# Optimization experiments

Measured on AMD Instinct MI355X. Metric: run time of the kernel, lower is better.

The kernel has to match this reference:

```python
import jax, jax.numpy as jnp
import numpy as np

N_IN, N_OUT, H, EMB, NSC = 32, 8, 256, 32, 5
B, T = 256, 512
D_IN0 = N_IN + N_OUT + EMB  # 72


def setup_inputs() -> dict:
    key = jax.random.key(0)
    ks = jax.random.split(key, 18)
    s = 0.05
    rn = lambda k, shape: (jax.random.normal(k, shape, jnp.float32) * s)
    return {
        "x_cv": jax.random.normal(ks[0], (B, T, N_IN), jnp.float32),
        "pv_init": jax.random.normal(ks[1], (B, N_OUT), jnp.float32),
        "scenario": jax.random.randint(ks[2], (B,), 0, NSC),
        "emb_table": rn(ks[3], (NSC, EMB)),
        "W_ih0": rn(ks[4], (4 * H, D_IN0)),
        "W_hh0": rn(ks[5], (4 * H, H)),
        "b_ih0": rn(ks[6], (4 * H,)),
        "b_hh0": rn(ks[7], (4 * H,)),
        "W_ih1": rn(ks[8], (4 * H, H)),
        "W_hh1": rn(ks[9], (4 * H, H)),
        "b_ih1": rn(ks[10], (4 * H,)),
        "b_hh1": rn(ks[11], (4 * H,)),
        "fc1_w": rn(ks[12], (H // 2, H)),
        "fc1_b": rn(ks[13], (H // 2,)),
        "fc2_w": rn(ks[14], (N_OUT, H // 2)),
        "fc2_b": rn(ks[15], (N_OUT,)),
    }


def _lstm_cell(x, h, c, W_ih, W_hh, b):
    # torch gate order: i, f, g, o
    g = x @ W_ih.T + h @ W_hh.T + b
    i, f, gg, o = jnp.split(g, 4, axis=-1)
    c_new = jax.nn.sigmoid(f) * c + jax.nn.sigmoid(i) * jnp.tanh(gg)
    h_new = jax.nn.sigmoid(o) * jnp.tanh(c_new)
    return h_new, c_new


def reference(x_cv, pv_init, scenario, emb_table, W_ih0, W_hh0, b_ih0, b_hh0,
              W_ih1, W_hh1, b_ih1, b_hh1, fc1_w, fc1_b, fc2_w, fc2_b):
    # previous prediction. Dropout inactive (eval mode).
    emb = emb_table[scenario]          # [B, EMB]
    b0 = b_ih0 + b_hh0
    b1 = b_ih1 + b_hh1
    Bsz = x_cv.shape[0]
    z = jnp.zeros((Bsz, H), x_cv.dtype)

    def step(carry, x_t):
        h0, c0, h1, c1, pv = carry
        xt = jnp.concatenate([x_t, pv, emb], axis=-1)   # [B, D_IN0]
        h0, c0 = _lstm_cell(xt, h0, c0, W_ih0, W_hh0, b0)
        h1, c1 = _lstm_cell(h0, h1, c1, W_ih1, W_hh1, b1)
        pv_pred = jax.nn.relu(h1 @ fc1_w.T + fc1_b) @ fc2_w.T + fc2_b
        new_carry = (h0, c0, h1, c1, jax.lax.stop_gradient(pv_pred))
        return new_carry, pv_pred

    init = (z, z, z, z, pv_init)
    _, outs = jax.lax.scan(step, init, jnp.swapaxes(x_cv, 0, 1))  # [T, B, N_OUT]
    return jnp.swapaxes(outs, 0, 1)  # [B, T, N_OUT]
```

## Files before the change

kernel.cpp:

```cpp
#include <hip/hip_runtime.h>
#include <hip/hip_bf16.h>


#define TSTEPS 512

typedef _Float16 h2 __attribute__((ext_vector_type(2)));
typedef unsigned long long ull;

#if __has_builtin(__builtin_amdgcn_fdot2)
#define FDOT2(a, b, c) __builtin_amdgcn_fdot2((a), (b), (c), false)
#else
#define FDOT2(a, b, c) ((c) + (float)(a).x * (float)(b).x + (float)(a).y * (float)(b).y)
#endif
#define BC(x) __builtin_bit_cast(h2, (x))

__device__ __forceinline__ float sigm(float x) { return 1.0f / (1.0f + __expf(-x)); }
__device__ __forceinline__ float tanhf_(float x) {
    float e = __expf(2.0f * x);
    return 1.0f - 2.0f / (e + 1.0f);
}

#define WQT_OFF 0u
#define HXA_OFF 1703936u
#define HXB_OFF 1966080u
#define FLG_OFF 2228224u
#define WS_NEED 2244608u

__device__ __forceinline__ float l0col(const float* __restrict__ Wih0,
                                       const float* __restrict__ Whh0, int row, int K) {
    if (K < 32) return Wih0[row * 72 + K];
    if (K < 288) return Whh0[row * 256 + (K - 32)];
    if (K < 296) return Wih0[row * 72 + 32 + (K - 288)];
    return 0.0f;
}

__global__ void prep_w(const float* __restrict__ Wih0, const float* __restrict__ Whh0,
                       const float* __restrict__ Wih1, const float* __restrict__ Whh1,
                       char* __restrict__ ws) {
    int gid = blockIdx.x * 256 + threadIdx.x;
    if (gid < 106496) {
        int q = gid % 52;
        int rest = gid / 52;
        int l = rest & 63, w = (rest >> 6) & 7, c = rest >> 9;
        float4 v;
        float* vp = (float*)&v;
#pragma unroll
        for (int gg = 0; gg < 4; ++gg) {
            int row = gg * 256 + c * 64 + l;
            float a0, a1;
            if (q < 20) {
                int K = w * 40 + q * 2;
                a0 = l0col(Wih0, Whh0, row, K);
                a1 = l0col(Wih0, Whh0, row, K + 1);
            } else if (q < 36) {
                int K = w * 32 + (q - 20) * 2;
                a0 = Wih1[row * 256 + K];
                a1 = Wih1[row * 256 + K + 1];
            } else {
                int K = w * 32 + (q - 36) * 2;
                a0 = Whh1[row * 256 + K];
                a1 = Whh1[row * 256 + K + 1];
            }
            h2 hv;
            hv.x = (_Float16)a0;
            hv.y = (_Float16)a1;
            vp[gg] = __builtin_bit_cast(float, hv);
        }
        ((float4*)ws)[gid] = v;
    } else {
        int z = gid - 106496;
        if (z < 4096) ((unsigned*)(ws + FLG_OFF))[z] = 0u;
    }
}

__device__ __forceinline__ void arrive(unsigned* cnt) {
    asm volatile("s_waitcnt vmcnt(0)" ::: "memory");
    __hip_atomic_fetch_add(cnt, 1u, __ATOMIC_RELAXED, __HIP_MEMORY_SCOPE_AGENT);
}
__device__ __forceinline__ void wait_cnt(unsigned* cnt, unsigned tgt) {
    while (__hip_atomic_load(cnt, __ATOMIC_RELAXED, __HIP_MEMORY_SCOPE_AGENT) < tgt)
        __builtin_amdgcn_s_sleep(1);
}
#define CBAR() asm volatile("" ::: "memory")

__device__ __forceinline__ void mac4(const float4& W, h2 x, float& r0, float& r1,
                                     float& r2, float& r3) {
    r0 = FDOT2(BC(W.x), x, r0);
    r1 = FDOT2(BC(W.y), x, r1);
    r2 = FDOT2(BC(W.z), x, r2);
    r3 = FDOT2(BC(W.w), x, r3);
}
__device__ __forceinline__ float dot8(const float4& W, const float4& X, float s) {
    s = FDOT2(BC(W.x), BC(X.x), s);
    s = FDOT2(BC(W.y), BC(X.y), s);
    s = FDOT2(BC(W.z), BC(X.z), s);
    s = FDOT2(BC(W.w), BC(X.w), s);
    return s;
}

__global__ __launch_bounds__(512) void lstm_main(
    const float* __restrict__ x_cv, const float* __restrict__ pv_init,
    const int* __restrict__ scen, const float* __restrict__ emb_table,
    const float* __restrict__ Wih0, const float* __restrict__ b_ih0,
    const float* __restrict__ b_hh0, const float* __restrict__ b_ih1,
    const float* __restrict__ b_hh1, const float* __restrict__ fc1_w,
    const float* __restrict__ fc1_b, const float* __restrict__ fc2_w,
    const float* __restrict__ fc2_b, char* __restrict__ ws,
    float* __restrict__ out) {
    struct __align__(16) SM {
        char fc1w[73856];
        char fc2w[2048];
        char xt0[4 * 640];
        char xt1[4 * 1024];
        float g0[4][256];
        float g1[4][256];
        float biasE[4][256];
        float bias1[256];
        unsigned short htmp[4][64];
        char fc1o[4 * 256];
        float embs[4][32];
        int scen_l[4];
    };
    __shared__ SM sm;

    const int tid = threadIdx.x;
    const int lane = tid & 63;
    const int wv = tid >> 6;
    const int c = blockIdx.x & 3;
    const int g = blockIdx.x >> 2;
    const int B0 = g * 4;

    ull* hxA = (ull*)(ws + HXA_OFF) + (unsigned)g * 512u;
    ull* hxB = (ull*)(ws + HXB_OFF) + (unsigned)g * 512u;
    unsigned* cntA = (unsigned*)(ws + FLG_OFF) + (unsigned)g * 32u;
    unsigned* cntB = cntA + 16;

    float4 wr[52];
    {
        const float4* wb = (const float4*)(ws + WQT_OFF) +
                           (unsigned)(((c * 8 + wv) * 64 + lane) * 52);
#pragma unroll
        for (int q = 0; q < 52; ++q) wr[q] = wb[q];
    }

    if (tid < 4) sm.scen_l[tid] = scen[B0 + tid];
    __syncthreads();

    if (tid < 128) {
        int b = tid >> 5, e = tid & 31;
        sm.embs[b][e] = emb_table[sm.scen_l[b] * 32 + e];
    }
    if (tid < 320) ((ull*)sm.xt0)[tid] = 0ull;
    ((ull*)sm.xt1)[tid] = 0ull;
    {
        int ks = tid & 3, row = tid >> 2;
        char* dst = sm.fc1w + ks * 18464 + row * 144;
        const float* src = fc1_w + row * 256 + ks * 64;
        for (int e = 0; e < 32; ++e) {
            h2 v;
            v.x = (_Float16)src[2 * e];
            v.y = (_Float16)src[2 * e + 1];
            *(h2*)(dst + e * 4) = v;
        }
    }
    {
        int jo = tid >> 6, ks = (tid >> 4) & 3, e = tid & 15;
        h2 v;
        v.x = (_Float16)fc2_w[jo * 128 + ks * 32 + 2 * e];
        v.y = (_Float16)fc2_w[jo * 128 + ks * 32 + 2 * e + 1];
        *(h2*)(sm.fc2w + (jo * 4 + ks) * 64 + e * 4) = v;
    }
    if (tid < 256) {
        int row = (tid >> 6) * 256 + c * 64 + (tid & 63);
        sm.bias1[tid] = b_ih1[row] + b_hh1[row];
    }
    __syncthreads();

    for (int idx = tid; idx < 1024; idx += 512) {
        int b = idx >> 8, r = idx & 255;
        int row = (r >> 6) * 256 + c * 64 + (r & 63);
        float s = b_ih0[row] + b_hh0[row];
        for (int e = 0; e < 32; ++e) s += sm.embs[b][e] * Wih0[row * 72 + 40 + e];
        sm.biasE[b][r] = s;
    }
    if (tid < 128) {
        int b = tid >> 5, k = tid & 31;
        float xv = x_cv[((size_t)(B0 + b) * TSTEPS + 0) * 32 + k];
        *(_Float16*)(sm.xt0 + b * 640 + k * 2) = (_Float16)xv;
    }
    if (tid < 32) {
        int b = tid >> 3, jo = tid & 7;
        *(_Float16*)(sm.xt0 + b * 640 + 576 + jo * 2) = (_Float16)pv_init[(B0 + b) * 8 + jo];
    }
    __syncthreads();

    for (int idx = tid; idx < 1024; idx += 512) {
        int b = idx >> 8, r = idx & 255;
        sm.g0[b][r] = sm.biasE[b][r];
        sm.g1[b][r] = sm.bias1[r];
    }
    const float fc1b_r = fc1_b[tid >> 2];
    const float fc2b_r = (tid < 128) ? fc2_b[(tid >> 2) & 7] : 0.0f;
    float c0 = 0.0f, c1 = 0.0f;
    __syncthreads();

    for (int t = 0; t < TSTEPS; ++t) {
        const int par = t & 1;
        const unsigned tgt = 4u * (unsigned)(t + 1);

        {
            float a0[4], a1[4], a2[4], a3[4];
#pragma unroll
            for (int b = 0; b < 4; ++b) a0[b] = a1[b] = a2[b] = a3[b] = 0.0f;
#pragma unroll
            for (int b = 0; b < 4; ++b) {
                const char* xb = sm.xt0 + b * 640 + wv * 80;
#pragma unroll
                for (int q = 0; q < 5; ++q) {
                    float4 xq = *(const float4*)(xb + q * 16);
                    mac4(wr[q * 4 + 0], BC(xq.x), a0[b], a1[b], a2[b], a3[b]);
                    mac4(wr[q * 4 + 1], BC(xq.y), a0[b], a1[b], a2[b], a3[b]);
                    mac4(wr[q * 4 + 2], BC(xq.z), a0[b], a1[b], a2[b], a3[b]);
                    mac4(wr[q * 4 + 3], BC(xq.w), a0[b], a1[b], a2[b], a3[b]);
                }
            }
#pragma unroll
            for (int b = 0; b < 4; ++b) {
                atomicAdd(&sm.g0[b][lane], a0[b]);
                atomicAdd(&sm.g0[b][64 + lane], a1[b]);
                atomicAdd(&sm.g0[b][128 + lane], a2[b]);
                atomicAdd(&sm.g0[b][192 + lane], a3[b]);
            }
        }
        __syncthreads();

        if (tid < 256) {
            int u = tid & 63, b = tid >> 6;
            float gi = sm.g0[b][u], gf = sm.g0[b][64 + u];
            float gc = sm.g0[b][128 + u], go = sm.g0[b][192 + u];
            c0 = sigm(gf) * c0 + sigm(gi) * tanhf_(gc);
            float h = sigm(go) * tanhf_(c0);
            sm.htmp[b][u] = __builtin_bit_cast(unsigned short, (_Float16)h);
        }
        __syncthreads();

        float b0a[4], b1a[4], b2a[4], b3a[4];
        if (wv == 0) {
            ull v = *(const ull*)((const char*)sm.htmp +
                                  ((lane >> 4) * 64 + (lane & 15) * 4) * 2);
            __hip_atomic_store(&hxA[(par * 4 + c) * 64 + lane], v, __ATOMIC_RELAXED,
                               __HIP_MEMORY_SCOPE_AGENT);
            if (lane == 0) arrive(cntA);
        }
        {
#pragma unroll
            for (int b = 0; b < 4; ++b) b0a[b] = b1a[b] = b2a[b] = b3a[b] = 0.0f;
#pragma unroll
            for (int b = 0; b < 4; ++b) {
                const char* xb = sm.xt1 + b * 1024 + 512 + wv * 64;
#pragma unroll
                for (int q = 0; q < 4; ++q) {
                    float4 xq = *(const float4*)(xb + q * 16);
                    mac4(wr[36 + q * 4 + 0], BC(xq.x), b0a[b], b1a[b], b2a[b], b3a[b]);
                    mac4(wr[36 + q * 4 + 1], BC(xq.y), b0a[b], b1a[b], b2a[b], b3a[b]);
                    mac4(wr[36 + q * 4 + 2], BC(xq.z), b0a[b], b1a[b], b2a[b], b3a[b]);
                    mac4(wr[36 + q * 4 + 3], BC(xq.w), b0a[b], b1a[b], b2a[b], b3a[b]);
                }
            }
        }
        for (int idx = tid; idx < 1024; idx += 512) {
            int b = idx >> 8, r = idx & 255;
            sm.g0[b][r] = sm.biasE[b][r];
        }
        if (tid == 0) wait_cnt(cntA, tgt);
        __syncthreads();
        CBAR();

        if (tid < 256) {
            int cc = tid >> 6, l = tid & 63;
            ull v = __hip_atomic_load(&hxA[(par * 4 + cc) * 64 + l], __ATOMIC_RELAXED,
                                      __HIP_MEMORY_SCOPE_AGENT);
            int b = l >> 4, ug = cc * 64 + (l & 15) * 4;
            *(ull*)(sm.xt1 + b * 1024 + ug * 2) = v;
            *(ull*)(sm.xt0 + b * 640 + 64 + ug * 2) = v;
        }
        __syncthreads();

        {
#pragma unroll
            for (int b = 0; b < 4; ++b) {
                const char* xb = sm.xt1 + b * 1024 + wv * 64;
#pragma unroll
                for (int q = 0; q < 4; ++q) {
                    float4 xq = *(const float4*)(xb + q * 16);
                    mac4(wr[20 + q * 4 + 0], BC(xq.x), b0a[b], b1a[b], b2a[b], b3a[b]);
                    mac4(wr[20 + q * 4 + 1], BC(xq.y), b0a[b], b1a[b], b2a[b], b3a[b]);
                    mac4(wr[20 + q * 4 + 2], BC(xq.z), b0a[b], b1a[b], b2a[b], b3a[b]);
                    mac4(wr[20 + q * 4 + 3], BC(xq.w), b0a[b], b1a[b], b2a[b], b3a[b]);
                }
            }
#pragma unroll
            for (int b = 0; b < 4; ++b) {
                atomicAdd(&sm.g1[b][lane], b0a[b]);
                atomicAdd(&sm.g1[b][64 + lane], b1a[b]);
                atomicAdd(&sm.g1[b][128 + lane], b2a[b]);
                atomicAdd(&sm.g1[b][192 + lane], b3a[b]);
            }
        }
        __syncthreads();

        if (tid < 256) {
            int u = tid & 63, b = tid >> 6;
            float gi = sm.g1[b][u], gf = sm.g1[b][64 + u];
            float gc = sm.g1[b][128 + u], go = sm.g1[b][192 + u];
            c1 = sigm(gf) * c1 + sigm(gi) * tanhf_(gc);
            float h = sigm(go) * tanhf_(c1);
            sm.htmp[b][u] = __builtin_bit_cast(unsigned short, (_Float16)h);
        }
        __syncthreads();

        if (wv == 0) {
            ull v = *(const ull*)((const char*)sm.htmp +
                                  ((lane >> 4) * 64 + (lane & 15) * 4) * 2);
            __hip_atomic_store(&hxB[(par * 4 + c) * 64 + lane], v, __ATOMIC_RELAXED,
                               __HIP_MEMORY_SCOPE_AGENT);
            if (lane == 0) arrive(cntB);
        }
        if (tid >= 128 && tid < 256 && t + 1 < TSTEPS) {
            int tt = tid - 128;
            int b = tt >> 5, k = tt & 31;
            float xv = x_cv[((size_t)(B0 + b) * TSTEPS + t + 1) * 32 + k];
            *(_Float16*)(sm.xt0 + b * 640 + k * 2) = (_Float16)xv;
        }
        for (int idx = tid; idx < 1024; idx += 512) {
            int b = idx >> 8, r = idx & 255;
            sm.g1[b][r] = sm.bias1[r];
        }
        if (tid == 0) wait_cnt(cntB, tgt);
        __syncthreads();
        CBAR();

        if (tid < 256) {
            int cc = tid >> 6, l = tid & 63;
            ull v = __hip_atomic_load(&hxB[(par * 4 + cc) * 64 + l], __ATOMIC_RELAXED,
                                      __HIP_MEMORY_SCOPE_AGENT);
            int b = l >> 4, ug = cc * 64 + (l & 15) * 4;
            *(ull*)(sm.xt1 + b * 1024 + 512 + ug * 2) = v;
        }
        __syncthreads();

        {
            const int fks = tid & 3, frow = tid >> 2;
            const char* wbase = sm.fc1w + fks * 18464 + frow * 144;
            float fa[4];
#pragma unroll
            for (int b = 0; b < 4; ++b) fa[b] = 0.0f;
#pragma unroll
            for (int b = 0; b < 4; ++b) {
                const char* xb = sm.xt1 + b * 1024 + 512 + fks * 128;
#pragma unroll
                for (int q = 0; q < 8; ++q) {
                    float4 W = *(const float4*)(wbase + q * 16);
                    float4 X = *(const float4*)(xb + q * 16);
                    fa[b] = dot8(W, X, fa[b]);
                }
            }
#pragma unroll
            for (int b = 0; b < 4; ++b) {
                float s = fa[b];
                s += __shfl_xor(s, 1);
                s += __shfl_xor(s, 2);
                if (fks == 0) {
                    float r = fmaxf(s + fc1b_r, 0.0f);
                    *(unsigned short*)(sm.fc1o + b * 256 + frow * 2) =
                        __builtin_bit_cast(unsigned short, (_Float16)r);
                }
            }
        }
        __syncthreads();

        if (tid < 128) {
            int ks = tid & 3, jo = (tid >> 2) & 7, b = tid >> 5;
            const char* wb2 = sm.fc2w + (jo * 4 + ks) * 64;
            const char* xb2 = sm.fc1o + b * 256 + ks * 64;
            float s = 0.0f;
#pragma unroll
            for (int q = 0; q < 4; ++q) {
                float4 W = *(const float4*)(wb2 + q * 16);
                float4 X = *(const float4*)(xb2 + q * 16);
                s = dot8(W, X, s);
            }
            s += __shfl_xor(s, 1);
            s += __shfl_xor(s, 2);
            if (ks == 0) {
                float pv = s + fc2b_r;
                *(_Float16*)(sm.xt0 + b * 640 + 576 + jo * 2) = (_Float16)pv;
                if (c == 0) out[((size_t)(B0 + b) * TSTEPS + t) * 8 + jo] = pv;
            }
        }
        __syncthreads();
    }
}

extern "C" void kernel_launch(void* const* d_in, const int* in_sizes, int n_in,
                              void* d_out, int out_size, void* d_ws, size_t ws_size,
                              hipStream_t stream) {
    if (ws_size < WS_NEED) return;

    const float* x_cv = (const float*)d_in[0];
    const float* pv_init = (const float*)d_in[1];
    const int* scen = (const int*)d_in[2];
    const float* embt = (const float*)d_in[3];
    const float* Wih0 = (const float*)d_in[4];
    const float* Whh0 = (const float*)d_in[5];
    const float* bih0 = (const float*)d_in[6];
    const float* bhh0 = (const float*)d_in[7];
    const float* Wih1 = (const float*)d_in[8];
    const float* Whh1 = (const float*)d_in[9];
    const float* bih1 = (const float*)d_in[10];
    const float* bhh1 = (const float*)d_in[11];
    const float* fc1w = (const float*)d_in[12];
    const float* fc1b = (const float*)d_in[13];
    const float* fc2w = (const float*)d_in[14];
    const float* fc2b = (const float*)d_in[15];

    char* ws = (char*)d_ws;

    prep_w<<<432, 256, 0, stream>>>(Wih0, Whh0, Wih1, Whh1, ws);

    lstm_main<<<256, 512, 0, stream>>>(x_cv, pv_init, scen, embt, Wih0, bih0, bhh0,
                                       bih1, bhh1, fc1w, fc1b, fc2w, fc2b, ws,
                                       (float*)d_out);
}
```

Baseline: 19.10 ms.

## Repartition LSTM across 8 blocks per batch group of 8 samples

Changes the grid decomposition from 4 hidden-unit slices times 4 samples per group to 8 slices of 32 units times 8 samples per group. Each thread now keeps half as many weight registers (26 float4 instead of 52) and computes packed dot8 products over 8 samples. fc1 weights are also cached in registers with a rotated index to avoid LDS bank conflicts. The goal is to cut register pressure and raise per-weight reuse, at the cost of a wider cross-block exchange (8 blocks per barrier) and more LDS atomics per step.

```diff
diff --git a/kernel.cpp b/kernel.cpp
--- a/kernel.cpp
+++ b/kernel.cpp
@@ -24,7 +24,7 @@
 #define HXA_OFF 1703936u
 #define HXB_OFF 1966080u
 #define FLG_OFF 2228224u
-#define WS_NEED 2244608u
+#define WS_NEED 2232320u
 
 __device__ __forceinline__ float l0col(const float* __restrict__ Wih0,
                                        const float* __restrict__ Whh0, int row, int K) {
@@ -39,37 +39,48 @@
                        char* __restrict__ ws) {
     int gid = blockIdx.x * 256 + threadIdx.x;
     if (gid < 106496) {
-        int q = gid % 52;
-        int rest = gid / 52;
+        int q = gid % 26;
+        int rest = gid / 26;
         int l = rest & 63, w = (rest >> 6) & 7, c = rest >> 9;
+        int gp = l >> 5, u = l & 31;
+        int r, K;
+        const float* base = nullptr;
+        if (q < 10) {
+            r = q / 5;
+            K = w * 40 + (q % 5) * 8;
+        } else if (q < 18) {
+            int z = q - 10;
+            r = z >> 2;
+            K = w * 32 + (z & 3) * 8;
+            base = Wih1;
+        } else {
+            int z = q - 18;
+            r = z >> 2;
+            K = w * 32 + (z & 3) * 8;
+            base = Whh1;
+        }
+        int row = (gp * 2 + r) * 256 + c * 32 + u;
         float4 v;
         float* vp = (float*)&v;
 #pragma unroll
-        for (int gg = 0; gg < 4; ++gg) {
-            int row = gg * 256 + c * 64 + l;
+        for (int e = 0; e < 4; ++e) {
             float a0, a1;
-            if (q < 20) {
-                int K = w * 40 + q * 2;
-                a0 = l0col(Wih0, Whh0, row, K);
-                a1 = l0col(Wih0, Whh0, row, K + 1);
-            } else if (q < 36) {
-                int K = w * 32 + (q - 20) * 2;
-                a0 = Wih1[row * 256 + K];
-                a1 = Wih1[row * 256 + K + 1];
+            if (base) {
+                a0 = base[row * 256 + K + 2 * e];
+                a1 = base[row * 256 + K + 2 * e + 1];
             } else {
-                int K = w * 32 + (q - 36) * 2;
-                a0 = Whh1[row * 256 + K];
-                a1 = Whh1[row * 256 + K + 1];
+                a0 = l0col(Wih0, Whh0, row, K + 2 * e);
+                a1 = l0col(Wih0, Whh0, row, K + 2 * e + 1);
             }
             h2 hv;
             hv.x = (_Float16)a0;
             hv.y = (_Float16)a1;
-            vp[gg] = __builtin_bit_cast(float, hv);
+            vp[e] = __builtin_bit_cast(float, hv);
         }
         ((float4*)ws)[gid] = v;
     } else {
         int z = gid - 106496;
-        if (z < 4096) ((unsigned*)(ws + FLG_OFF))[z] = 0u;
+        if (z < 1024) ((unsigned*)(ws + FLG_OFF))[z] = 0u;
     }
 }
 
@@ -83,13 +94,6 @@
 }
 #define CBAR() asm volatile("" ::: "memory")
 
-__device__ __forceinline__ void mac4(const float4& W, h2 x, float& r0, float& r1,
-                                     float& r2, float& r3) {
-    r0 = FDOT2(BC(W.x), x, r0);
-    r1 = FDOT2(BC(W.y), x, r1);
-    r2 = FDOT2(BC(W.z), x, r2);
-    r3 = FDOT2(BC(W.w), x, r3);
-}
 __device__ __forceinline__ float dot8(const float4& W, const float4& X, float s) {
     s = FDOT2(BC(W.x), BC(X.x), s);
     s = FDOT2(BC(W.y), BC(X.y), s);
@@ -98,7 +102,7 @@
     return s;
 }
 
-__global__ __launch_bounds__(512) void lstm_main(
+__global__ __launch_bounds__(512, 2) void lstm_main(
     const float* __restrict__ x_cv, const float* __restrict__ pv_init,
     const int* __restrict__ scen, const float* __restrict__ emb_table,
     const float* __restrict__ Wih0, const float* __restrict__ b_ih0,
@@ -108,294 +112,282 @@
     const float* __restrict__ fc2_b, char* __restrict__ ws,
     float* __restrict__ out) {
     struct __align__(16) SM {
-        char fc1w[73856];
+        char fc1w[4 * 16400];
         char fc2w[2048];
-        char xt0[4 * 640];
-        char xt1[4 * 1024];
-        float g0[4][256];
-        float g1[4][256];
-        float biasE[4][256];
-        float bias1[256];
-        unsigned short htmp[4][64];
-        char fc1o[4 * 256];
-        float embs[4][32];
-        int scen_l[4];
+        char xt0[8 * 640];
+        char xt1[8 * 1024];
+        float g0[8][128];
+        float g1[8][128];
+        float biasE[8][128];
+        float bias1[128];
+        unsigned short htmp[8][32];
+        char fc1o[8 * 256];
+        float embs[8][32];
+        int scen_l[8];
     };
     __shared__ SM sm;
 
     const int tid = threadIdx.x;
     const int lane = tid & 63;
     const int wv = tid >> 6;
-    const int c = blockIdx.x & 3;
-    const int g = blockIdx.x >> 2;
-    const int B0 = g * 4;
-
-    ull* hxA = (ull*)(ws + HXA_OFF) + (unsigned)g * 512u;
-    ull* hxB = (ull*)(ws + HXB_OFF) + (unsigned)g * 512u;
+    const int c = blockIdx.x & 7;
+    const int g = blockIdx.x >> 3;
+    const int B0 = g * 8;
+    const int gp = lane >> 5, u = lane & 31;
+
+    ull* hxA = (ull*)(ws + HXA_OFF) + (unsigned)g * 1024u;
+    ull* hxB = (ull*)(ws + HXB_OFF) + (unsigned)g * 1024u;
     unsigned* cntA = (unsigned*)(ws + FLG_OFF) + (unsigned)g * 32u;
     unsigned* cntB = cntA + 16;
 
-    float4 wr[52];
+    float4 wr[26];
     {
         const float4* wb = (const float4*)(ws + WQT_OFF) +
-                           (unsigned)(((c * 8 + wv) * 64 + lane) * 52);
-#pragma unroll
-        for (int q = 0; q < 52; ++q) wr[q] = wb[q];
-    }
-
-    if (tid < 4) sm.scen_l[tid] = scen[B0 + tid];
+                           (unsigned)(((c * 8 + wv) * 64 + lane) * 26);
+#pragma unroll
+        for (int q = 0; q < 26; ++q) wr[q] = wb[q];
+    }
+
+    if (tid < 8) sm.scen_l[tid] = scen[B0 + tid];
     __syncthreads();
-
-    if (tid < 128) {
+    if (tid < 256) {
         int b = tid >> 5, e = tid & 31;
         sm.embs[b][e] = emb_table[sm.scen_l[b] * 32 + e];
     }
-    if (tid < 320) ((ull*)sm.xt0)[tid] = 0ull;
-    ((ull*)sm.xt1)[tid] = 0ull;
+    for (int idx = tid; idx < 640; idx += 512) ((ull*)sm.xt0)[idx] = 0ull;
+    for (int idx = tid; idx < 1024; idx += 512) ((ull*)sm.xt1)[idx] = 0ull;
     {
         int ks = tid & 3, row = tid >> 2;
-        char* dst = sm.fc1w + ks * 18464 + row * 144;
-        const float* src = fc1_w + row * 256 + ks * 64;
-        for (int e = 0; e < 32; ++e) {
-            h2 v;
-            v.x = (_Float16)src[2 * e];
-            v.y = (_Float16)src[2 * e + 1];
-            *(h2*)(dst + e * 4) = v;
-        }
-    }
-    {
-        int jo = tid >> 6, ks = (tid >> 4) & 3, e = tid & 15;
-        h2 v;
-        v.x = (_Float16)fc2_w[jo * 128 + ks * 32 + 2 * e];
-        v.y = (_Float16)fc2_w[jo * 128 + ks * 32 + 2 * e + 1];
-        *(h2*)(sm.fc2w + (jo * 4 + ks) * 64 + e * 4) = v;
-    }
-    if (tid < 256) {
-        int row = (tid >> 6) * 256 + c * 64 + (tid & 63);
+        for (int q = 0; q < 8; ++q) {
+            const float* src = fc1_w + row * 256 + ks * 64 + q * 8;
+            char* dst = sm.fc1w + ks * 16400 + q * 2048 + row * 16;
+#pragma unroll
+            for (int e = 0; e < 4; ++e) {
+                h2 v;
+                v.x = (_Float16)src[2 * e];
+                v.y = (_Float16)src[2 * e + 1];
+                *(h2*)(dst + e * 4) = v;
+            }
+        }
+    }
+    if (tid < 128) {
+        int jo = tid >> 4, ks = (tid >> 2) & 3, e4 = tid & 3;
+        float4 v;
+        float* vp = (float*)&v;
+#pragma unroll
+        for (int e = 0; e < 4; ++e) {
+            h2 hv;
+            hv.x = (_Float16)fc2_w[jo * 128 + ks * 32 + e4 * 8 + 2 * e];
+            hv.y = (_Float16)fc2_w[jo * 128 + ks * 32 + e4 * 8 + 2 * e + 1];
+            vp[e] = __builtin_bit_cast(float, hv);
+        }
+        *(float4*)(sm.fc2w + (jo * 4 + ks) * 64 + e4 * 16) = v;
+    }
+    if (tid < 128) {
+        int row = (tid >> 5) * 256 + c * 32 + (tid & 31);
         sm.bias1[tid] = b_ih1[row] + b_hh1[row];
     }
     __syncthreads();
-
     for (int idx = tid; idx < 1024; idx += 512) {
-        int b = idx >> 8, r = idx & 255;
-        int row = (r >> 6) * 256 + c * 64 + (r & 63);
+        int b = idx >> 7, r = idx & 127;
+        int row = (r >> 5) * 256 + c * 32 + (r & 31);
         float s = b_ih0[row] + b_hh0[row];
         for (int e = 0; e < 32; ++e) s += sm.embs[b][e] * Wih0[row * 72 + 40 + e];
         sm.biasE[b][r] = s;
     }
-    if (tid < 128) {
+    if (tid < 256) {
         int b = tid >> 5, k = tid & 31;
         float xv = x_cv[((size_t)(B0 + b) * TSTEPS + 0) * 32 + k];
         *(_Float16*)(sm.xt0 + b * 640 + k * 2) = (_Float16)xv;
     }
-    if (tid < 32) {
+    if (tid < 64) {
         int b = tid >> 3, jo = tid & 7;
         *(_Float16*)(sm.xt0 + b * 640 + 576 + jo * 2) = (_Float16)pv_init[(B0 + b) * 8 + jo];
     }
     __syncthreads();
-
     for (int idx = tid; idx < 1024; idx += 512) {
-        int b = idx >> 8, r = idx & 255;
+        int b = idx >> 7, r = idx & 127;
         sm.g0[b][r] = sm.biasE[b][r];
         sm.g1[b][r] = sm.bias1[r];
     }
-    const float fc1b_r = fc1_b[tid >> 2];
-    const float fc2b_r = (tid < 128) ? fc2_b[(tid >> 2) & 7] : 0.0f;
+    const int f_ks = tid & 3, f_row = tid >> 2;
+    const float fc1b_r = fc1_b[f_row];
+    const int ks2 = tid & 3, jo = (tid >> 2) & 7, bo = tid >> 5;
+    const float fc2b_r = (tid < 256) ? fc2_b[jo] : 0.0f;
+    float4 f1w[8];
+#pragma unroll
+    for (int i = 0; i < 8; ++i) {
+        int qx = (i + 2 * f_ks) & 7;
+        f1w[i] = *(const float4*)(sm.fc1w + f_ks * 16400 + qx * 2048 + f_row * 16);
+    }
     float c0 = 0.0f, c1 = 0.0f;
     __syncthreads();
 
     for (int t = 0; t < TSTEPS; ++t) {
         const int par = t & 1;
-        const unsigned tgt = 4u * (unsigned)(t + 1);
-
-        {
-            float a0[4], a1[4], a2[4], a3[4];
-#pragma unroll
-            for (int b = 0; b < 4; ++b) a0[b] = a1[b] = a2[b] = a3[b] = 0.0f;
-#pragma unroll
-            for (int b = 0; b < 4; ++b) {
+        const unsigned tgt = 8u * (unsigned)(t + 1);
+
+        {
+            float a0[8], a1[8];
+#pragma unroll
+            for (int b = 0; b < 8; ++b) a0[b] = a1[b] = 0.0f;
+#pragma unroll
+            for (int b = 0; b < 8; ++b) {
                 const char* xb = sm.xt0 + b * 640 + wv * 80;
 #pragma unroll
                 for (int q = 0; q < 5; ++q) {
                     float4 xq = *(const float4*)(xb + q * 16);
-                    mac4(wr[q * 4 + 0], BC(xq.x), a0[b], a1[b], a2[b], a3[b]);
-                    mac4(wr[q * 4 + 1], BC(xq.y), a0[b], a1[b], a2[b], a3[b]);
-                    mac4(wr[q * 4 + 2], BC(xq.z), a0[b], a1[b], a2[b], a3[b]);
-                    mac4(wr[q * 4 + 3], BC(xq.w), a0[b], a1[b], a2[b], a3[b]);
+                    a0[b] = dot8(wr[q], xq, a0[b]);
+                    a1[b] = dot8(wr[5 + q], xq, a1[b]);
                 }
             }
 #pragma unroll
-            for (int b = 0; b < 4; ++b) {
-                atomicAdd(&sm.g0[b][lane], a0[b]);
-                atomicAdd(&sm.g0[b][64 + lane], a1[b]);
-                atomicAdd(&sm.g0[b][128 + lane], a2[b]);
-                atomicAdd(&sm.g0[b][192 + lane], a3[b]);
+            for (int b = 0; b < 8; ++b) {
+                atomicAdd(&sm.g0[b][gp * 64 + u], a0[b]);
+                atomicAdd(&sm.g0[b][gp * 64 + 32 + u], a1[b]);
             }
         }
         __syncthreads();
 
         if (tid < 256) {
-            int u = tid & 63, b = tid >> 6;
-            float gi = sm.g0[b][u], gf = sm.g0[b][64 + u];
-            float gc = sm.g0[b][128 + u], go = sm.g0[b][192 + u];
+            int uu = tid & 31, b = tid >> 5;
+            float gi = sm.g0[b][uu], gf = sm.g0[b][32 + uu];
+            float gc = sm.g0[b][64 + uu], go = sm.g0[b][96 + uu];
             c0 = sigm(gf) * c0 + sigm(gi) * tanhf_(gc);
-            float h = sigm(go) * tanhf_(c0);
-            sm.htmp[b][u] = __builtin_bit_cast(unsigned short, (_Float16)h);
-        }
-        __syncthreads();
-
-        float b0a[4], b1a[4], b2a[4], b3a[4];
+            sm.htmp[b][uu] = __builtin_bit_cast(unsigned short, (_Float16)(sigm(go) * tanhf_(c0)));
+        }
+        __syncthreads();
+
+        float e0[8], e1[8];
         if (wv == 0) {
-            ull v = *(const ull*)((const char*)sm.htmp +
-                                  ((lane >> 4) * 64 + (lane & 15) * 4) * 2);
-            __hip_atomic_store(&hxA[(par * 4 + c) * 64 + lane], v, __ATOMIC_RELAXED,
+            ull v = ((const ull*)sm.htmp)[lane];
+            __hip_atomic_store(&hxA[(par * 8 + c) * 64 + lane], v, __ATOMIC_RELAXED,
                                __HIP_MEMORY_SCOPE_AGENT);
             if (lane == 0) arrive(cntA);
         }
         {
 #pragma unroll
-            for (int b = 0; b < 4; ++b) b0a[b] = b1a[b] = b2a[b] = b3a[b] = 0.0f;
-#pragma unroll
-            for (int b = 0; b < 4; ++b) {
+            for (int b = 0; b < 8; ++b) e0[b] = e1[b] = 0.0f;
+#pragma unroll
+            for (int b = 0; b < 8; ++b) {
                 const char* xb = sm.xt1 + b * 1024 + 512 + wv * 64;
 #pragma unroll
                 for (int q = 0; q < 4; ++q) {
                     float4 xq = *(const float4*)(xb + q * 16);
-                    mac4(wr[36 + q * 4 + 0], BC(xq.x), b0a[b], b1a[b], b2a[b], b3a[b]);
-                    mac4(wr[36 + q * 4 + 1], BC(xq.y), b0a[b], b1a[b], b2a[b], b3a[b]);
-                    mac4(wr[36 + q * 4 + 2], BC(xq.z), b0a[b], b1a[b], b2a[b], b3a[b]);
-                    mac4(wr[36 + q * 4 + 3], BC(xq.w), b0a[b], b1a[b], b2a[b], b3a[b]);
+                    e0[b] = dot8(wr[18 + q], xq, e0[b]);
+                    e1[b] = dot8(wr[22 + q], xq, e1[b]);
                 }
             }
         }
         for (int idx = tid; idx < 1024; idx += 512) {
-            int b = idx >> 8, r = idx & 255;
+            int b = idx >> 7, r = idx & 127;
             sm.g0[b][r] = sm.biasE[b][r];
         }
         if (tid == 0) wait_cnt(cntA, tgt);
         __syncthreads();
         CBAR();
 
-        if (tid < 256) {
+        {
             int cc = tid >> 6, l = tid & 63;
-            ull v = __hip_atomic_load(&hxA[(par * 4 + cc) * 64 + l], __ATOMIC_RELAXED,
+            ull v = __hip_atomic_load(&hxA[(par * 8 + cc) * 64 + l], __ATOMIC_RELAXED,
                                       __HIP_MEMORY_SCOPE_AGENT);
-            int b = l >> 4, ug = cc * 64 + (l & 15) * 4;
-            *(ull*)(sm.xt1 + b * 1024 + ug * 2) = v;
-            *(ull*)(sm.xt0 + b * 640 + 64 + ug * 2) = v;
-        }
-        __syncthreads();
-
-        {
-#pragma unroll
-            for (int b = 0; b < 4; ++b) {
+            int b = l >> 3, u4 = cc * 32 + (l & 7) * 4;
+            *(ull*)(sm.xt1 + b * 1024 + u4 * 2) = v;
+            *(ull*)(sm.xt0 + b * 640 + 64 + u4 * 2) = v;
+        }
+        __syncthreads();
+
+        {
+#pragma unroll
+            for (int b = 0; b < 8; ++b) {
                 const char* xb = sm.xt1 + b * 1024 + wv * 64;
 #pragma unroll
                 for (int q = 0; q < 4; ++q) {
                     float4 xq = *(const float4*)(xb + q * 16);
-                    mac4(wr[20 + q * 4 + 0], BC(xq.x), b0a[b], b1a[b], b2a[b], b3a[b]);
-                    mac4(wr[20 + q * 4 + 1], BC(xq.y), b0a[b], b1a[b], b2a[b], b3a[b]);
-                    mac4(wr[20 + q * 4 + 2], BC(xq.z), b0a[b], b1a[b], b2a[b], b3a[b]);
-                    mac4(wr[20 + q * 4 + 3], BC(xq.w), b0a[b], b1a[b], b2a[b], b3a[b]);
+                    e0[b] = dot8(wr[10 + q], xq, e0[b]);
+                    e1[b] = dot8(wr[14 + q], xq, e1[b]);
                 }
             }
 #pragma unroll
-            for (int b = 0; b < 4; ++b) {
-                atomicAdd(&sm.g1[b][lane], b0a[b]);
-                atomicAdd(&sm.g1[b][64 + lane], b1a[b]);
-                atomicAdd(&sm.g1[b][128 + lane], b2a[b]);
-                atomicAdd(&sm.g1[b][192 + lane], b3a[b]);
+            for (int b = 0; b < 8; ++b) {
+                atomicAdd(&sm.g1[b][gp * 64 + u], e0[b]);
+                atomicAdd(&sm.g1[b][gp * 64 + 32 + u], e1[b]);
             }
         }
         __syncthreads();
 
         if (tid < 256) {
-            int u = tid & 63, b = tid >> 6;
-            float gi = sm.g1[b][u], gf = sm.g1[b][64 + u];
-            float gc = sm.g1[b][128 + u], go = sm.g1[b][192 + u];
+            int uu = tid & 31, b = tid >> 5;
+            float gi = sm.g1[b][uu], gf = sm.g1[b][32 + uu];
+            float gc = sm.g1[b][64 + uu], go = sm.g1[b][96 + uu];
             c1 = sigm(gf) * c1 + sigm(gi) * tanhf_(gc);
-            float h = sigm(go) * tanhf_(c1);
-            sm.htmp[b][u] = __builtin_bit_cast(unsigned short, (_Float16)h);
+            sm.htmp[b][uu] = __builtin_bit_cast(unsigned short, (_Float16)(sigm(go) * tanhf_(c1)));
         }
         __syncthreads();
 
         if (wv == 0) {
-            ull v = *(const ull*)((const char*)sm.htmp +
-                                  ((lane >> 4) * 64 + (lane & 15) * 4) * 2);
-            __hip_atomic_store(&hxB[(par * 4 + c) * 64 + lane], v, __ATOMIC_RELAXED,
+            ull v = ((const ull*)sm.htmp)[lane];
+            __hip_atomic_store(&hxB[(par * 8 + c) * 64 + lane], v, __ATOMIC_RELAXED,
                                __HIP_MEMORY_SCOPE_AGENT);
             if (lane == 0) arrive(cntB);
         }
-        if (tid >= 128 && tid < 256 && t + 1 < TSTEPS) {
-            int tt = tid - 128;
+        if (tid >= 256 && t + 1 < TSTEPS) {
+            int tt = tid - 256;
             int b = tt >> 5, k = tt & 31;
             float xv = x_cv[((size_t)(B0 + b) * TSTEPS + t + 1) * 32 + k];
             *(_Float16*)(sm.xt0 + b * 640 + k * 2) = (_Float16)xv;
         }
         for (int idx = tid; idx < 1024; idx += 512) {
-            int b = idx >> 8, r = idx & 255;
+            int b = idx >> 7, r = idx & 127;
             sm.g1[b][r] = sm.bias1[r];
         }
         if (tid == 0) wait_cnt(cntB, tgt);
         __syncthreads();
         CBAR();
 
-        if (tid < 256) {
+        {
             int cc = tid >> 6, l = tid & 63;
-            ull v = __hip_atomic_load(&hxB[(par * 4 + cc) * 64 + l], __ATOMIC_RELAXED,
+            ull v = __hip_atomic_load(&hxB[(par * 8 + cc) * 64 + l], __ATOMIC_RELAXED,
                                       __HIP_MEMORY_SCOPE_AGENT);
-            int b = l >> 4, ug = cc * 64 + (l & 15) * 4;
-            *(ull*)(sm.xt1 + b * 1024 + 512 + ug * 2) = v;
-        }
-        __syncthreads();
-
-        {
-            const int fks = tid & 3, frow = tid >> 2;
-            const char* wbase = sm.fc1w + fks * 18464 + frow * 144;
-            float fa[4];
-#pragma unroll
-            for (int b = 0; b < 4; ++b) fa[b] = 0.0f;
-#pragma unroll
-            for (int b = 0; b < 4; ++b) {
-                const char* xb = sm.xt1 + b * 1024 + 512 + fks * 128;
-#pragma unroll
-                for (int q = 0; q < 8; ++q) {
-                    float4 W = *(const float4*)(wbase + q * 16);
-                    float4 X = *(const float4*)(xb + q * 16);
-                    fa[b] = dot8(W, X, fa[b]);
+            int b = l >> 3, u4 = cc * 32 + (l & 7) * 4;
+            *(ull*)(sm.xt1 + b * 1024 + 512 + u4 * 2) = v;
+        }
+        __syncthreads();
+
+        {
+#pragma unroll
+            for (int b = 0; b < 8; ++b) {
+                float a = 0.0f;
+                const char* xb = sm.xt1 + b * 1024 + 512 + f_ks * 128;
+#pragma unroll
+                for (int i = 0; i < 8; ++i) {
+                    int qx = (i + 2 * f_ks) & 7;
+                    a = dot8(f1w[i], *(const float4*)(xb + qx * 16), a);
                 }
-            }
-#pragma unroll
-            for (int b = 0; b < 4; ++b) {
-                float s = fa[b];
-                s += __shfl_xor(s, 1);
-                s += __shfl_xor(s, 2);
-                if (fks == 0) {
-                    float r = fmaxf(s + fc1b_r, 0.0f);
-                    *(unsigned short*)(sm.fc1o + b * 256 + frow * 2) =
+                a += __shfl_xor(a, 1);
+                a += __shfl_xor(a, 2);
+                if (f_ks == 0) {
+                    float r = fmaxf(a + fc1b_r, 0.0f);
+                    *(unsigned short*)(sm.fc1o + b * 256 + f_row * 2) =
                         __builtin_bit_cast(unsigned short, (_Float16)r);
                 }
             }
         }
         __syncthreads();
 
-        if (tid < 128) {
-            int ks = tid & 3, jo = (tid >> 2) & 7, b = tid >> 5;
-            const char* wb2 = sm.fc2w + (jo * 4 + ks) * 64;
-            const char* xb2 = sm.fc1o + b * 256 + ks * 64;
+        if (tid < 256) {
+            const char* wb2 = sm.fc2w + (jo * 4 + ks2) * 64;
+            const char* xb2 = sm.fc1o + bo * 256 + ks2 * 64;
             float s = 0.0f;
 #pragma unroll
-            for (int q = 0; q < 4; ++q) {
-                float4 W = *(const float4*)(wb2 + q * 16);
-                float4 X = *(const float4*)(xb2 + q * 16);
-                s = dot8(W, X, s);
-            }
+            for (int q = 0; q < 4; ++q)
+                s = dot8(*(const float4*)(wb2 + q * 16), *(const float4*)(xb2 + q * 16), s);
             s += __shfl_xor(s, 1);
             s += __shfl_xor(s, 2);
-            if (ks == 0) {
+            if (ks2 == 0) {
                 float pv = s + fc2b_r;
-                *(_Float16*)(sm.xt0 + b * 640 + 576 + jo * 2) = (_Float16)pv;
-                if (c == 0) out[((size_t)(B0 + b) * TSTEPS + t) * 8 + jo] = pv;
+                *(_Float16*)(sm.xt0 + bo * 640 + 576 + jo * 2) = (_Float16)pv;
+                if (c == 0) out[((size_t)(B0 + bo) * TSTEPS + t) * 8 + jo] = pv;
             }
         }
         __syncthreads();
@@ -426,7 +418,7 @@
 
     char* ws = (char*)d_ws;
 
-    prep_w<<<432, 256, 0, stream>>>(Wih0, Whh0, Wih1, Whh1, ws);
+    prep_w<<<420, 256, 0, stream>>>(Wih0, Whh0, Wih1, Whh1, ws);
 
     lstm_main<<<256, 512, 0, stream>>>(x_cv, pv_init, scen, embt, Wih0, bih0, bhh0,
                                        bih1, bhh1, fc1w, fc1b, fc2w, fc2b, ws,
```

Measured after the change: 21.04 ms. 10.1% more time.
